# Performance work log

Hardware: AMD Instinct MI355X
Metric: run time of the kernel (lower is better)

The kernel has to match this reference:

```python
import jax, jax.numpy as jnp
import numpy as np

B, S, H = 2, 2048, 2048
E, I, K = 32, 768, 8
NORM_TOPK = True


def setup_inputs() -> dict:
    key = jax.random.key(0)
    k0, k1, k2, k3, k4 = jax.random.split(key, 5)
    scale = 0.02
    return {
        "hidden_states": jax.random.normal(k0, (B, S, H), dtype=jnp.float32),
        "w_router": jax.random.normal(k1, (E, H), dtype=jnp.float32) * scale,   # gate.weight [E,H]
        "w_gate": jax.random.normal(k2, (E, I, H), dtype=jnp.float32) * scale,  # gate_proj per expert
        "w_up": jax.random.normal(k3, (E, I, H), dtype=jnp.float32) * scale,    # up_proj per expert
        "w_down": jax.random.normal(k4, (E, H, I), dtype=jnp.float32) * scale,  # down_proj per expert
    }


def reference(hidden_states, w_router, w_gate, w_up, w_down):
    b, s, h = hidden_states.shape
    x = hidden_states.reshape(-1, h)                       # [T, H]
    T = x.shape[0]

    router_logits = x @ w_router.T                         # [T, E]
    probs = jax.nn.softmax(router_logits.astype(jnp.float32), axis=-1)
    topk_w, topk_idx = jax.lax.top_k(probs, K)             # [T, K]
    if NORM_TOPK:
        topk_w = topk_w / jnp.sum(topk_w, axis=-1, keepdims=True)

    # Scatter top-k weights into a dense combine matrix [T, E]
    combine = jnp.zeros((T, w_router.shape[0]), dtype=jnp.float32)
    combine = combine.at[jnp.arange(T)[:, None], topk_idx].add(topk_w)

    # SwiGLU MLP per expert, combined with routing weights
    g = jnp.einsum('th,eih->tei', x, w_gate)               # [T, E, I]
    u = jnp.einsum('th,eih->tei', x, w_up)                 # [T, E, I]
    act = jax.nn.silu(g) * u                               # [T, E, I]
    act = act * combine[:, :, None]                        # weight before down-proj
    out = jnp.einsum('tei,ehi->th', act, w_down)           # [T, H]

    out = out.reshape(b, s, h).astype(hidden_states.dtype)
    return out, router_logits.reshape(b, s, -1)
```

## Files before the change

kernel.cpp:

```cpp
#include <hip/hip_runtime.h>
#include <hip/hip_bf16.h>

#define T_TOK 4096
#define H_DIM 2048
#define E_EXP 32
#define I_DIM 768
#define K_TOP 8
#define TOTAL_ROWS (T_TOK * K_TOP)

typedef __attribute__((ext_vector_type(8))) short bfrag;
typedef __attribute__((ext_vector_type(4))) float f32x4;

static __device__ __forceinline__ unsigned short f2bf(float f) {
  unsigned int x = __float_as_uint(f);
  x += 0x7FFFu + ((x >> 16) & 1u);
  return (unsigned short)(x >> 16);
}
static __device__ __forceinline__ unsigned int pack2(float a, float b) {
  return (unsigned int)f2bf(a) | ((unsigned int)f2bf(b) << 16);
}

#if __has_builtin(__builtin_amdgcn_global_load_lds)
typedef __attribute__((address_space(1))) const unsigned int as1_u32;
typedef __attribute__((address_space(3))) unsigned int as3_u32;
static __device__ __forceinline__ void gll16(const unsigned short* g, unsigned short* l) {
  __builtin_amdgcn_global_load_lds((as1_u32*)g, (as3_u32*)l, 16, 0, 0);
}
#else
static __device__ __forceinline__ void gll16(const unsigned short* g, unsigned short* l) {
  uint4 v = *(const uint4*)g;
  ((uint4*)l)[threadIdx.x & 63] = v;
}
#endif

__global__ __launch_bounds__(256) void cast_f32_bf16_kernel(const float* __restrict__ s,
                                                            unsigned short* __restrict__ d,
                                                            long long n8) {
  long long i = (long long)blockIdx.x * 256 + threadIdx.x;
  if (i >= n8) return;
  const float4* sp = (const float4*)s;
  float4 a = sp[2 * i], b = sp[2 * i + 1];
  uint4 o;
  o.x = pack2(a.x, a.y); o.y = pack2(a.z, a.w);
  o.z = pack2(b.x, b.y); o.w = pack2(b.z, b.w);
  ((uint4*)d)[i] = o;
}

__global__ __launch_bounds__(256) void router_kernel(
    const float* __restrict__ x, const float* __restrict__ wr,
    float* __restrict__ logits_out, int* __restrict__ tok_list,
    float* __restrict__ wgt_list, int* __restrict__ cnt) {
  __shared__ float xs[4][H_DIM];
  __shared__ float lg[4][E_EXP];
  const int tid = threadIdx.x;
  const int t0 = blockIdx.x * 4;

  const float4* src = (const float4*)(x + (size_t)t0 * H_DIM);
  float4* dst = (float4*)&xs[0][0];
  for (int i = tid; i < 4 * H_DIM / 4; i += 256) dst[i] = src[i];
  __syncthreads();

  const int g = tid >> 3, l8 = tid & 7;
  float a0 = 0.f, a1 = 0.f, a2 = 0.f, a3 = 0.f;
  const float* w = wr + (size_t)g * H_DIM;
  for (int c = l8; c < H_DIM; c += 8) {
    float wv = w[c];
    a0 += xs[0][c] * wv; a1 += xs[1][c] * wv;
    a2 += xs[2][c] * wv; a3 += xs[3][c] * wv;
  }
  #pragma unroll
  for (int m = 4; m; m >>= 1) {
    a0 += __shfl_xor(a0, m); a1 += __shfl_xor(a1, m);
    a2 += __shfl_xor(a2, m); a3 += __shfl_xor(a3, m);
  }
  if (l8 == 0) { lg[0][g] = a0; lg[1][g] = a1; lg[2][g] = a2; lg[3][g] = a3; }
  __syncthreads();

  if (tid < 128) {
    int r = tid >> 5, e = tid & 31;
    logits_out[(size_t)(t0 + r) * E_EXP + e] = lg[r][e];
  }

  if (tid < 4) {
    int t = t0 + tid;
    unsigned sel = 0;
    float lv[K_TOP]; int ei[K_TOP];
    #pragma unroll
    for (int k = 0; k < K_TOP; ++k) {
      float best = -3.4e38f; int bi = 0;
      for (int e = 0; e < E_EXP; ++e) {
        float v = lg[tid][e];
        if (!((sel >> e) & 1u) && v > best) { best = v; bi = e; }
      }
      sel |= 1u << bi; lv[k] = best; ei[k] = bi;
    }
    float m = lv[0], se = 0.f, ex[K_TOP];
    #pragma unroll
    for (int k = 0; k < K_TOP; ++k) { ex[k] = __expf(lv[k] - m); se += ex[k]; }
    float inv = 1.f / se;
    #pragma unroll
    for (int k = 0; k < K_TOP; ++k) {
      int e = ei[k];
      int pos = atomicAdd(&cnt[e], 1);
      tok_list[e * T_TOK + pos] = t;
      wgt_list[e * T_TOK + pos] = ex[k] * inv;
    }
  }
}

__global__ void scan_kernel(const int* __restrict__ cnt, int* __restrict__ aoff) {
  if (threadIdx.x == 0 && blockIdx.x == 0) {
    int s = 0;
    for (int e = 0; e < E_EXP; ++e) { aoff[e] = s; s += cnt[e]; }
  }
}


__global__ __launch_bounds__(256) void gateup_kernel(
    const unsigned short* __restrict__ xb,
    const unsigned short* __restrict__ wgb, const unsigned short* __restrict__ wub,
    const int* __restrict__ cnt, const int* __restrict__ aoff,
    const int* __restrict__ tok_list, const float* __restrict__ wgt_list,
    unsigned short* __restrict__ act) {
  const int bx = blockIdx.x;
  const int cb = bx % 6;
  const int t  = bx / 6;
  const int e  = t >> 5, rb = t & 31;
  const int nt = cnt[e];
  const int row0 = rb * 128;
  if (row0 >= nt) return;
  const int n0 = cb * 128;

  __shared__ __align__(16) unsigned short As[128 * 64];
  __shared__ __align__(16) unsigned short Bgs[128 * 64];
  __shared__ __align__(16) unsigned short Bus[128 * 64];
  __shared__ int toks[128];
  __shared__ float wrow[128];

  const int tid = threadIdx.x;
  if (tid < 128) {
    int r = row0 + tid;
    bool v = r < nt;
    toks[tid] = v ? tok_list[e * T_TOK + r] : 0;
    wrow[tid] = v ? wgt_list[e * T_TOK + r] : 0.f;
  }
  __syncthreads();

  const int rr = tid >> 3, c8 = tid & 7;
  const unsigned short* pa[4];
  const unsigned short* pbg[4];
  #pragma unroll
  for (int j = 0; j < 4; ++j) {
    int r = j * 32 + rr;
    int c = 8 * (c8 ^ (r & 7));
    pa[j]  = xb + (size_t)toks[r] * H_DIM + c;
    pbg[j] = wgb + ((size_t)e * I_DIM + n0 + r) * H_DIM + c;
  }
  const size_t du = (size_t)(wub - wgb);

  f32x4 zero = {0.f, 0.f, 0.f, 0.f};
  f32x4 ag[4][4], au[4][4];
  #pragma unroll
  for (int m = 0; m < 4; ++m)
    #pragma unroll
    for (int n = 0; n < 4; ++n) { ag[m][n] = zero; au[m][n] = zero; }

  const int lane = tid & 63;
  const int w = tid >> 6;
  const int wr = (w >> 1) * 64, wc = (w & 1) * 64;
  const int lbase = w * 512;

  for (int kt = 0; kt < H_DIM; kt += 64) {
    #pragma unroll
    for (int j = 0; j < 4; ++j) gll16(pa[j] + kt,       &As[j * 2048 + lbase]);
    #pragma unroll
    for (int j = 0; j < 4; ++j) gll16(pbg[j] + kt,      &Bgs[j * 2048 + lbase]);
    #pragma unroll
    for (int j = 0; j < 4; ++j) gll16(pbg[j] + du + kt, &Bus[j * 2048 + lbase]);
    __syncthreads();
    #pragma unroll
    for (int kk = 0; kk < 2; ++kk) {
      bfrag a[4], bg[4], bu[4];
      #pragma unroll
      for (int m = 0; m < 4; ++m) {
        int r = wr + m * 16 + (lane & 15);
        int el = (r * 64 + kk * 32 + (lane >> 4) * 8) ^ ((r & 7) << 3);
        a[m] = *(const bfrag*)&As[el];
      }
      #pragma unroll
      for (int n = 0; n < 4; ++n) {
        int r = wc + n * 16 + (lane & 15);
        int el = (r * 64 + kk * 32 + (lane >> 4) * 8) ^ ((r & 7) << 3);
        bg[n] = *(const bfrag*)&Bgs[el];
        bu[n] = *(const bfrag*)&Bus[el];
      }
      #pragma unroll
      for (int m = 0; m < 4; ++m)
        #pragma unroll
        for (int n = 0; n < 4; ++n) {
          ag[m][n] = __builtin_amdgcn_mfma_f32_16x16x32_bf16(a[m], bg[n], ag[m][n], 0, 0, 0);
          au[m][n] = __builtin_amdgcn_mfma_f32_16x16x32_bf16(a[m], bu[n], au[m][n], 0, 0, 0);
        }
    }
    __syncthreads();
  }

  const int aoe = aoff[e];
  #pragma unroll
  for (int m = 0; m < 4; ++m) {
    #pragma unroll
    for (int r4 = 0; r4 < 4; ++r4) {
      int rloc = wr + m * 16 + (lane >> 4) * 4 + r4;
      int grow = row0 + rloc;
      if (grow < nt) {
        float wgt = wrow[rloc];
        size_t base = (size_t)(aoe + grow) * I_DIM + n0 + wc + (lane & 15);
        #pragma unroll
        for (int n = 0; n < 4; ++n) {
          float g = ag[m][n][r4], u = au[m][n][r4];
          float s = g / (1.f + __expf(-g));
          act[base + n * 16] = f2bf(s * u * wgt);
        }
      }
    }
  }
}

__global__ __launch_bounds__(256) void down_kernel(
    const unsigned short* __restrict__ act, const unsigned short* __restrict__ wdb,
    const int* __restrict__ cnt, const int* __restrict__ aoff,
    const int* __restrict__ tok_list, float* __restrict__ out) {
  const int bx = blockIdx.x;
  const int cb = bx & 15;
  const int t  = bx >> 4;
  const int e  = t >> 5, rb = t & 31;
  const int nt = cnt[e];
  const int row0 = rb * 128;
  if (row0 >= nt) return;
  const int h0 = cb * 128;

  __shared__ __align__(16) unsigned short As[128 * 64];
  __shared__ __align__(16) unsigned short Bd[128 * 64];
  __shared__ int toks[128];

  const int tid = threadIdx.x;
  const int aoe = aoff[e];
  if (tid < 128) {
    int r = row0 + tid;
    toks[tid] = (r < nt) ? tok_list[e * T_TOK + r] : 0;
  }
  __syncthreads();

  const int rr = tid >> 3, c8 = tid & 7;
  const unsigned short* pa[4];
  const unsigned short* pb[4];
  #pragma unroll
  for (int j = 0; j < 4; ++j) {
    int r = j * 32 + rr;
    int c = 8 * (c8 ^ (r & 7));
    int arow = aoe + row0 + r;
    if (arow > TOTAL_ROWS - 1) arow = TOTAL_ROWS - 1;
    pa[j] = act + (size_t)arow * I_DIM + c;
    pb[j] = wdb + ((size_t)e * H_DIM + h0 + r) * I_DIM + c;
  }

  f32x4 zero = {0.f, 0.f, 0.f, 0.f};
  f32x4 acc[4][4];
  #pragma unroll
  for (int m = 0; m < 4; ++m)
    #pragma unroll
    for (int n = 0; n < 4; ++n) acc[m][n] = zero;

  const int lane = tid & 63;
  const int w = tid >> 6;
  const int wr = (w >> 1) * 64, wc = (w & 1) * 64;
  const int lbase = w * 512;

  for (int kt = 0; kt < I_DIM; kt += 64) {
    #pragma unroll
    for (int j = 0; j < 4; ++j) gll16(pa[j] + kt, &As[j * 2048 + lbase]);
    #pragma unroll
    for (int j = 0; j < 4; ++j) gll16(pb[j] + kt, &Bd[j * 2048 + lbase]);
    __syncthreads();
    #pragma unroll
    for (int kk = 0; kk < 2; ++kk) {
      bfrag a[4], b[4];
      #pragma unroll
      for (int m = 0; m < 4; ++m) {
        int r = wr + m * 16 + (lane & 15);
        int el = (r * 64 + kk * 32 + (lane >> 4) * 8) ^ ((r & 7) << 3);
        a[m] = *(const bfrag*)&As[el];
      }
      #pragma unroll
      for (int n = 0; n < 4; ++n) {
        int r = wc + n * 16 + (lane & 15);
        int el = (r * 64 + kk * 32 + (lane >> 4) * 8) ^ ((r & 7) << 3);
        b[n] = *(const bfrag*)&Bd[el];
      }
      #pragma unroll
      for (int m = 0; m < 4; ++m)
        #pragma unroll
        for (int n = 0; n < 4; ++n)
          acc[m][n] = __builtin_amdgcn_mfma_f32_16x16x32_bf16(a[m], b[n], acc[m][n], 0, 0, 0);
    }
    __syncthreads();
  }

  #pragma unroll
  for (int m = 0; m < 4; ++m) {
    #pragma unroll
    for (int r4 = 0; r4 < 4; ++r4) {
      int rloc = wr + m * 16 + (lane >> 4) * 4 + r4;
      int grow = row0 + rloc;
      if (grow < nt) {
        int tok = toks[rloc];
        size_t base = (size_t)tok * H_DIM + h0 + wc + (lane & 15);
        #pragma unroll
        for (int n = 0; n < 4; ++n)
          atomicAdd(out + base + n * 16, acc[m][n][r4]);
      }
    }
  }
}

__global__ __launch_bounds__(256) void gateup_fb(
    const unsigned short* __restrict__ xb,
    const float* __restrict__ wg, const float* __restrict__ wu,
    const int* __restrict__ cnt, const int* __restrict__ aoff,
    const int* __restrict__ tok_list, const float* __restrict__ wgt_list,
    unsigned short* __restrict__ act) {
  const int e = blockIdx.x >> 5;
  const int rb = blockIdx.x & 31;
  const int nt = cnt[e];
  const int row0 = rb * 128;
  if (row0 >= nt) return;
  const int n0 = blockIdx.y * 128;

  __shared__ __align__(16) unsigned short As[128 * 64];
  __shared__ __align__(16) unsigned short Bgs[128 * 64];
  __shared__ __align__(16) unsigned short Bus[128 * 64];
  __shared__ int toks[128];
  __shared__ float wrow[128];

  const int tid = threadIdx.x;
  if (tid < 128) {
    int r = row0 + tid;
    bool v = r < nt;
    toks[tid] = v ? tok_list[e * T_TOK + r] : 0;
    wrow[tid] = v ? wgt_list[e * T_TOK + r] : 0.f;
  }

  f32x4 zero = {0.f, 0.f, 0.f, 0.f};
  f32x4 ag[4][4], au[4][4];
  #pragma unroll
  for (int m = 0; m < 4; ++m)
    #pragma unroll
    for (int n = 0; n < 4; ++n) { ag[m][n] = zero; au[m][n] = zero; }

  const int lane = tid & 63;
  const int wv = tid >> 6;
  const int wr = (wv >> 1) * 64;
  const int wc = (wv & 1) * 64;

  const float* wgp = wg + ((size_t)e * I_DIM + n0) * H_DIM;
  const float* wup = wu + ((size_t)e * I_DIM + n0) * H_DIM;

  for (int kt = 0; kt < H_DIM; kt += 64) {
    __syncthreads();
    #pragma unroll
    for (int i = 0; i < 4; ++i) {
      int q = tid + 256 * i;
      int r = q >> 3, cc = q & 7;
      uint4 av = *(const uint4*)(xb + (size_t)toks[r] * H_DIM + (kt + cc * 8));
      int el = (r * 64 + cc * 8) ^ ((r & 7) << 3);
      *(uint4*)&As[el] = av;
    }
    #pragma unroll
    for (int i = 0; i < 4; ++i) {
      int q = tid + 256 * i;
      int r = q >> 3, cc = q & 7;
      size_t off = (size_t)r * H_DIM + (kt + cc * 8);
      float4 g0 = *(const float4*)(wgp + off);
      float4 g1 = *(const float4*)(wgp + off + 4);
      float4 u0 = *(const float4*)(wup + off);
      float4 u1 = *(const float4*)(wup + off + 4);
      int el = (r * 64 + cc * 8) ^ ((r & 7) << 3);
      uint4 pg, pu;
      pg.x = pack2(g0.x, g0.y); pg.y = pack2(g0.z, g0.w);
      pg.z = pack2(g1.x, g1.y); pg.w = pack2(g1.z, g1.w);
      pu.x = pack2(u0.x, u0.y); pu.y = pack2(u0.z, u0.w);
      pu.z = pack2(u1.x, u1.y); pu.w = pack2(u1.z, u1.w);
      *(uint4*)&Bgs[el] = pg;
      *(uint4*)&Bus[el] = pu;
    }
    __syncthreads();
    #pragma unroll
    for (int kk = 0; kk < 2; ++kk) {
      bfrag a[4], bg[4], bu[4];
      #pragma unroll
      for (int m = 0; m < 4; ++m) {
        int r = wr + m * 16 + (lane & 15);
        int el = (r * 64 + kk * 32 + (lane >> 4) * 8) ^ ((r & 7) << 3);
        a[m] = *(const bfrag*)&As[el];
      }
      #pragma unroll
      for (int n = 0; n < 4; ++n) {
        int r = wc + n * 16 + (lane & 15);
        int el = (r * 64 + kk * 32 + (lane >> 4) * 8) ^ ((r & 7) << 3);
        bg[n] = *(const bfrag*)&Bgs[el];
        bu[n] = *(const bfrag*)&Bus[el];
      }
      #pragma unroll
      for (int m = 0; m < 4; ++m)
        #pragma unroll
        for (int n = 0; n < 4; ++n) {
          ag[m][n] = __builtin_amdgcn_mfma_f32_16x16x32_bf16(a[m], bg[n], ag[m][n], 0, 0, 0);
          au[m][n] = __builtin_amdgcn_mfma_f32_16x16x32_bf16(a[m], bu[n], au[m][n], 0, 0, 0);
        }
    }
  }

  const int aoe = aoff[e];
  #pragma unroll
  for (int m = 0; m < 4; ++m) {
    #pragma unroll
    for (int r4 = 0; r4 < 4; ++r4) {
      int rloc = wr + m * 16 + (lane >> 4) * 4 + r4;
      int grow = row0 + rloc;
      if (grow < nt) {
        float wgt = wrow[rloc];
        size_t base = (size_t)(aoe + grow) * I_DIM + n0 + wc + (lane & 15);
        #pragma unroll
        for (int n = 0; n < 4; ++n) {
          float g = ag[m][n][r4];
          float u = au[m][n][r4];
          float s = g / (1.f + __expf(-g));
          act[base + n * 16] = f2bf(s * u * wgt);
        }
      }
    }
  }
}

__global__ __launch_bounds__(256) void down_fb(
    const unsigned short* __restrict__ act, const float* __restrict__ wd,
    const int* __restrict__ cnt, const int* __restrict__ aoff,
    const int* __restrict__ tok_list, float* __restrict__ out) {
  const int e = blockIdx.x >> 5;
  const int rb = blockIdx.x & 31;
  const int nt = cnt[e];
  const int row0 = rb * 128;
  if (row0 >= nt) return;
  const int h0 = blockIdx.y * 128;

  __shared__ __align__(16) unsigned short As[128 * 64];
  __shared__ __align__(16) unsigned short Bd[128 * 64];
  __shared__ int toks[128];

  const int tid = threadIdx.x;
  const int aoe = aoff[e];
  if (tid < 128) {
    int r = row0 + tid;
    toks[tid] = (r < nt) ? tok_list[e * T_TOK + r] : 0;
  }

  f32x4 zero = {0.f, 0.f, 0.f, 0.f};
  f32x4 acc[4][4];
  #pragma unroll
  for (int m = 0; m < 4; ++m)
    #pragma unroll
    for (int n = 0; n < 4; ++n) acc[m][n] = zero;

  const int lane = tid & 63;
  const int wv = tid >> 6;
  const int wr = (wv >> 1) * 64;
  const int wc = (wv & 1) * 64;

  const float* wdp = wd + ((size_t)e * H_DIM + h0) * I_DIM;

  for (int kt = 0; kt < I_DIM; kt += 64) {
    __syncthreads();
    #pragma unroll
    for (int i = 0; i < 4; ++i) {
      int q = tid + 256 * i;
      int r = q >> 3, cc = q & 7;
      int arow = aoe + row0 + r;
      if (arow > TOTAL_ROWS - 1) arow = TOTAL_ROWS - 1;
      uint4 av = *(const uint4*)(act + (size_t)arow * I_DIM + (kt + cc * 8));
      int el = (r * 64 + cc * 8) ^ ((r & 7) << 3);
      *(uint4*)&As[el] = av;
    }
    #pragma unroll
    for (int i = 0; i < 4; ++i) {
      int q = tid + 256 * i;
      int r = q >> 3, cc = q & 7;
      size_t off = (size_t)r * I_DIM + (kt + cc * 8);
      float4 b0 = *(const float4*)(wdp + off);
      float4 b1 = *(const float4*)(wdp + off + 4);
      int el = (r * 64 + cc * 8) ^ ((r & 7) << 3);
      uint4 pb;
      pb.x = pack2(b0.x, b0.y); pb.y = pack2(b0.z, b0.w);
      pb.z = pack2(b1.x, b1.y); pb.w = pack2(b1.z, b1.w);
      *(uint4*)&Bd[el] = pb;
    }
    __syncthreads();
    #pragma unroll
    for (int kk = 0; kk < 2; ++kk) {
      bfrag a[4], b[4];
      #pragma unroll
      for (int m = 0; m < 4; ++m) {
        int r = wr + m * 16 + (lane & 15);
        int el = (r * 64 + kk * 32 + (lane >> 4) * 8) ^ ((r & 7) << 3);
        a[m] = *(const bfrag*)&As[el];
      }
      #pragma unroll
      for (int n = 0; n < 4; ++n) {
        int r = wc + n * 16 + (lane & 15);
        int el = (r * 64 + kk * 32 + (lane >> 4) * 8) ^ ((r & 7) << 3);
        b[n] = *(const bfrag*)&Bd[el];
      }
      #pragma unroll
      for (int m = 0; m < 4; ++m)
        #pragma unroll
        for (int n = 0; n < 4; ++n)
          acc[m][n] = __builtin_amdgcn_mfma_f32_16x16x32_bf16(a[m], b[n], acc[m][n], 0, 0, 0);
    }
  }

  #pragma unroll
  for (int m = 0; m < 4; ++m) {
    #pragma unroll
    for (int r4 = 0; r4 < 4; ++r4) {
      int rloc = wr + m * 16 + (lane >> 4) * 4 + r4;
      int grow = row0 + rloc;
      if (grow < nt) {
        int tok = toks[rloc];
        size_t base = (size_t)tok * H_DIM + h0 + wc + (lane & 15);
        #pragma unroll
        for (int n = 0; n < 4; ++n)
          atomicAdd(out + base + n * 16, acc[m][n][r4]);
      }
    }
  }
}

extern "C" void kernel_launch(void* const* d_in, const int* in_sizes, int n_in,
                              void* d_out, int out_size, void* d_ws, size_t ws_size,
                              hipStream_t stream) {
  const float* x  = (const float*)d_in[0];
  const float* wr = (const float*)d_in[1];
  const float* wg = (const float*)d_in[2];
  const float* wu = (const float*)d_in[3];
  const float* wd = (const float*)d_in[4];
  float* out = (float*)d_out;
  float* logits_out = out + (size_t)T_TOK * H_DIM;

  const long long WELEM = (long long)E_EXP * I_DIM * H_DIM;
  const size_t WBYT = (size_t)WELEM * 2;

  const size_t XB_OFF  = 0;
  const size_t WGB_OFF = 16777216;
  const size_t WUB_OFF = WGB_OFF + WBYT;
  const size_t WDB_OFF = WUB_OFF + WBYT;
  const size_t TOK_OFF = WDB_OFF + WBYT;
  const size_t WGT_OFF = TOK_OFF + 524288;
  const size_t CNT_OFF = WGT_OFF + 524288;
  const size_t AOF_OFF = CNT_OFF + 256;
  const size_t ACT_OFF = AOF_OFF + 256;
  const size_t NEED    = ACT_OFF + (size_t)TOTAL_ROWS * I_DIM * 2;

  char* ws = (char*)d_ws;
  hipMemsetAsync(out, 0, (size_t)T_TOK * H_DIM * sizeof(float), stream);

  if (ws_size >= NEED) {
    unsigned short* xb  = (unsigned short*)(ws + XB_OFF);
    unsigned short* wgb = (unsigned short*)(ws + WGB_OFF);
    unsigned short* wub = (unsigned short*)(ws + WUB_OFF);
    unsigned short* wdb = (unsigned short*)(ws + WDB_OFF);
    int*   tok_list = (int*)(ws + TOK_OFF);
    float* wgt_list = (float*)(ws + WGT_OFF);
    int*   cnt  = (int*)(ws + CNT_OFF);
    int*   aoff = (int*)(ws + AOF_OFF);
    unsigned short* act = (unsigned short*)(ws + ACT_OFF);

    hipMemsetAsync(cnt, 0, 256, stream);
    cast_f32_bf16_kernel<<<4096, 256, 0, stream>>>(x, xb, (long long)T_TOK * H_DIM / 8);
    cast_f32_bf16_kernel<<<24576, 256, 0, stream>>>(wg, wgb, WELEM / 8);
    cast_f32_bf16_kernel<<<24576, 256, 0, stream>>>(wu, wub, WELEM / 8);
    cast_f32_bf16_kernel<<<24576, 256, 0, stream>>>(wd, wdb, WELEM / 8);
    router_kernel<<<T_TOK / 4, 256, 0, stream>>>(x, wr, logits_out, tok_list, wgt_list, cnt);
    scan_kernel<<<1, 64, 0, stream>>>(cnt, aoff);
    gateup_kernel<<<E_EXP * 32 * 6, 256, 0, stream>>>(
        xb, wgb, wub, cnt, aoff, tok_list, wgt_list, act);
    down_kernel<<<E_EXP * 32 * 16, 256, 0, stream>>>(
        act, wdb, cnt, aoff, tok_list, out);
  } else {
    unsigned short* xb   = (unsigned short*)ws;
    int*   tok_list      = (int*)(ws + 16777216);
    float* wgt_list      = (float*)(ws + 16777216 + 524288);
    int*   cnt           = (int*)(ws + 16777216 + 1048576);
    int*   aoff          = (int*)(ws + 16777216 + 1048576 + 256);
    unsigned short* act  = (unsigned short*)(ws + 16777216 + 1048576 + 512);

    hipMemsetAsync(cnt, 0, 256, stream);
    cast_f32_bf16_kernel<<<4096, 256, 0, stream>>>(x, xb, (long long)T_TOK * H_DIM / 8);
    router_kernel<<<T_TOK / 4, 256, 0, stream>>>(x, wr, logits_out, tok_list, wgt_list, cnt);
    scan_kernel<<<1, 64, 0, stream>>>(cnt, aoff);
    gateup_fb<<<dim3(E_EXP * 32, I_DIM / 128), 256, 0, stream>>>(
        xb, wg, wu, cnt, aoff, tok_list, wgt_list, act);
    down_fb<<<dim3(E_EXP * 32, H_DIM / 128), 256, 0, stream>>>(
        act, wd, cnt, aoff, tok_list, out);
  }
}
```

Baseline: 1.483 ms.

## Double-buffer LDS in MoE GEMMs, shrink gate-up N tile, reorder block mapping

After: 2.315 ms. 56.1% more time.

```diff
diff --git a/kernel.cpp b/kernel.cpp
--- a/kernel.cpp
+++ b/kernel.cpp
@@ -123,86 +123,91 @@
     const int* __restrict__ tok_list, const float* __restrict__ wgt_list,
     unsigned short* __restrict__ act) {
   const int bx = blockIdx.x;
-  const int cb = bx % 6;
-  const int t  = bx / 6;
-  const int e  = t >> 5, rb = t & 31;
+  const int rb = bx & 31;
+  const int q  = bx >> 5;
+  const int cb = q % 12;
+  const int e  = q / 12;
   const int nt = cnt[e];
   const int row0 = rb * 128;
   if (row0 >= nt) return;
-  const int n0 = cb * 128;
-
-  __shared__ __align__(16) unsigned short As[128 * 64];
-  __shared__ __align__(16) unsigned short Bgs[128 * 64];
-  __shared__ __align__(16) unsigned short Bus[128 * 64];
-  __shared__ int toks[128];
-  __shared__ float wrow[128];
+  const int n0 = cb * 64;
+
+  __shared__ __align__(16) unsigned short lds[2][16384];
 
   const int tid = threadIdx.x;
-  if (tid < 128) {
-    int r = row0 + tid;
-    bool v = r < nt;
-    toks[tid] = v ? tok_list[e * T_TOK + r] : 0;
-    wrow[tid] = v ? wgt_list[e * T_TOK + r] : 0.f;
-  }
-  __syncthreads();
-
   const int rr = tid >> 3, c8 = tid & 7;
+
   const unsigned short* pa[4];
-  const unsigned short* pbg[4];
+  const unsigned short* pbg[2];
   #pragma unroll
   for (int j = 0; j < 4; ++j) {
     int r = j * 32 + rr;
-    int c = 8 * (c8 ^ (r & 7));
-    pa[j]  = xb + (size_t)toks[r] * H_DIM + c;
-    pbg[j] = wgb + ((size_t)e * I_DIM + n0 + r) * H_DIM + c;
+    int gr = row0 + r;
+    int tok = (gr < nt) ? tok_list[e * T_TOK + gr] : 0;
+    pa[j] = xb + (size_t)tok * H_DIM + 8 * (c8 ^ (r & 7));
+  }
+  #pragma unroll
+  for (int j = 0; j < 2; ++j) {
+    int r = j * 32 + rr;
+    pbg[j] = wgb + ((size_t)e * I_DIM + n0 + r) * H_DIM + 8 * (c8 ^ (r & 7));
   }
   const size_t du = (size_t)(wub - wgb);
 
   f32x4 zero = {0.f, 0.f, 0.f, 0.f};
-  f32x4 ag[4][4], au[4][4];
+  f32x4 ag[4][2], au[4][2];
   #pragma unroll
   for (int m = 0; m < 4; ++m)
     #pragma unroll
-    for (int n = 0; n < 4; ++n) { ag[m][n] = zero; au[m][n] = zero; }
+    for (int n = 0; n < 2; ++n) { ag[m][n] = zero; au[m][n] = zero; }
 
   const int lane = tid & 63;
   const int w = tid >> 6;
-  const int wr = (w >> 1) * 64, wc = (w & 1) * 64;
+  const int wr = (w >> 1) * 64;
+  const int wc = (w & 1) * 32;
   const int lbase = w * 512;
 
+  auto STAGE = [&](int b, int kt) {
+    #pragma unroll
+    for (int j = 0; j < 4; ++j) gll16(pa[j] + kt,       &lds[b][j * 2048 + lbase]);
+    #pragma unroll
+    for (int j = 0; j < 2; ++j) gll16(pbg[j] + kt,      &lds[b][8192 + j * 2048 + lbase]);
+    #pragma unroll
+    for (int j = 0; j < 2; ++j) gll16(pbg[j] + du + kt, &lds[b][12288 + j * 2048 + lbase]);
+  };
+
+  int cur = 0;
+  STAGE(0, 0);
+  __syncthreads();
+
   for (int kt = 0; kt < H_DIM; kt += 64) {
-    #pragma unroll
-    for (int j = 0; j < 4; ++j) gll16(pa[j] + kt,       &As[j * 2048 + lbase]);
-    #pragma unroll
-    for (int j = 0; j < 4; ++j) gll16(pbg[j] + kt,      &Bgs[j * 2048 + lbase]);
-    #pragma unroll
-    for (int j = 0; j < 4; ++j) gll16(pbg[j] + du + kt, &Bus[j * 2048 + lbase]);
-    __syncthreads();
+    int nxt = kt + 64;
+    if (nxt < H_DIM) STAGE(cur ^ 1, nxt);
     #pragma unroll
     for (int kk = 0; kk < 2; ++kk) {
-      bfrag a[4], bg[4], bu[4];
+      bfrag a[4], bg[2], bu[2];
       #pragma unroll
       for (int m = 0; m < 4; ++m) {
         int r = wr + m * 16 + (lane & 15);
         int el = (r * 64 + kk * 32 + (lane >> 4) * 8) ^ ((r & 7) << 3);
-        a[m] = *(const bfrag*)&As[el];
-      }
-      #pragma unroll
-      for (int n = 0; n < 4; ++n) {
+        a[m] = *(const bfrag*)&lds[cur][el];
+      }
+      #pragma unroll
+      for (int n = 0; n < 2; ++n) {
         int r = wc + n * 16 + (lane & 15);
         int el = (r * 64 + kk * 32 + (lane >> 4) * 8) ^ ((r & 7) << 3);
-        bg[n] = *(const bfrag*)&Bgs[el];
-        bu[n] = *(const bfrag*)&Bus[el];
+        bg[n] = *(const bfrag*)&lds[cur][8192 + el];
+        bu[n] = *(const bfrag*)&lds[cur][12288 + el];
       }
       #pragma unroll
       for (int m = 0; m < 4; ++m)
         #pragma unroll
-        for (int n = 0; n < 4; ++n) {
+        for (int n = 0; n < 2; ++n) {
           ag[m][n] = __builtin_amdgcn_mfma_f32_16x16x32_bf16(a[m], bg[n], ag[m][n], 0, 0, 0);
           au[m][n] = __builtin_amdgcn_mfma_f32_16x16x32_bf16(a[m], bu[n], au[m][n], 0, 0, 0);
         }
     }
     __syncthreads();
+    cur ^= 1;
   }
 
   const int aoe = aoff[e];
@@ -213,10 +218,10 @@
       int rloc = wr + m * 16 + (lane >> 4) * 4 + r4;
       int grow = row0 + rloc;
       if (grow < nt) {
-        float wgt = wrow[rloc];
+        float wgt = wgt_list[e * T_TOK + grow];
         size_t base = (size_t)(aoe + grow) * I_DIM + n0 + wc + (lane & 15);
         #pragma unroll
-        for (int n = 0; n < 4; ++n) {
+        for (int n = 0; n < 2; ++n) {
           float g = ag[m][n][r4], u = au[m][n][r4];
           float s = g / (1.f + __expf(-g));
           act[base + n * 16] = f2bf(s * u * wgt);
@@ -231,27 +236,21 @@
     const int* __restrict__ cnt, const int* __restrict__ aoff,
     const int* __restrict__ tok_list, float* __restrict__ out) {
   const int bx = blockIdx.x;
-  const int cb = bx & 15;
-  const int t  = bx >> 4;
-  const int e  = t >> 5, rb = t & 31;
+  const int rb = bx & 31;
+  const int q  = bx >> 5;
+  const int cb = q & 15;
+  const int e  = q >> 4;
   const int nt = cnt[e];
   const int row0 = rb * 128;
   if (row0 >= nt) return;
   const int h0 = cb * 128;
 
-  __shared__ __align__(16) unsigned short As[128 * 64];
-  __shared__ __align__(16) unsigned short Bd[128 * 64];
-  __shared__ int toks[128];
+  __shared__ __align__(16) unsigned short lds[2][16384];
 
   const int tid = threadIdx.x;
   const int aoe = aoff[e];
-  if (tid < 128) {
-    int r = row0 + tid;
-    toks[tid] = (r < nt) ? tok_list[e * T_TOK + r] : 0;
-  }
-  __syncthreads();
-
   const int rr = tid >> 3, c8 = tid & 7;
+
   const unsigned short* pa[4];
   const unsigned short* pb[4];
   #pragma unroll
@@ -276,12 +275,20 @@
   const int wr = (w >> 1) * 64, wc = (w & 1) * 64;
   const int lbase = w * 512;
 
+  auto STAGE = [&](int b, int kt) {
+    #pragma unroll
+    for (int j = 0; j < 4; ++j) gll16(pa[j] + kt, &lds[b][j * 2048 + lbase]);
+    #pragma unroll
+    for (int j = 0; j < 4; ++j) gll16(pb[j] + kt, &lds[b][8192 + j * 2048 + lbase]);
+  };
+
+  int cur = 0;
+  STAGE(0, 0);
+  __syncthreads();
+
   for (int kt = 0; kt < I_DIM; kt += 64) {
-    #pragma unroll
-    for (int j = 0; j < 4; ++j) gll16(pa[j] + kt, &As[j * 2048 + lbase]);
-    #pragma unroll
-    for (int j = 0; j < 4; ++j) gll16(pb[j] + kt, &Bd[j * 2048 + lbase]);
-    __syncthreads();
+    int nxt = kt + 64;
+    if (nxt < I_DIM) STAGE(cur ^ 1, nxt);
     #pragma unroll
     for (int kk = 0; kk < 2; ++kk) {
       bfrag a[4], b[4];
@@ -289,13 +296,13 @@
       for (int m = 0; m < 4; ++m) {
         int r = wr + m * 16 + (lane & 15);
         int el = (r * 64 + kk * 32 + (lane >> 4) * 8) ^ ((r & 7) << 3);
-        a[m] = *(const bfrag*)&As[el];
+        a[m] = *(const bfrag*)&lds[cur][el];
       }
       #pragma unroll
       for (int n = 0; n < 4; ++n) {
         int r = wc + n * 16 + (lane & 15);
         int el = (r * 64 + kk * 32 + (lane >> 4) * 8) ^ ((r & 7) << 3);
-        b[n] = *(const bfrag*)&Bd[el];
+        b[n] = *(const bfrag*)&lds[cur][8192 + el];
       }
       #pragma unroll
       for (int m = 0; m < 4; ++m)
@@ -304,6 +311,7 @@
           acc[m][n] = __builtin_amdgcn_mfma_f32_16x16x32_bf16(a[m], b[n], acc[m][n], 0, 0, 0);
     }
     __syncthreads();
+    cur ^= 1;
   }
 
   #pragma unroll
@@ -313,7 +321,7 @@
       int rloc = wr + m * 16 + (lane >> 4) * 4 + r4;
       int grow = row0 + rloc;
       if (grow < nt) {
-        int tok = toks[rloc];
+        int tok = tok_list[e * T_TOK + grow];
         size_t base = (size_t)tok * H_DIM + h0 + wc + (lane & 15);
         #pragma unroll
         for (int n = 0; n < 4; ++n)
@@ -590,9 +598,9 @@
     cast_f32_bf16_kernel<<<24576, 256, 0, stream>>>(wd, wdb, WELEM / 8);
     router_kernel<<<T_TOK / 4, 256, 0, stream>>>(x, wr, logits_out, tok_list, wgt_list, cnt);
     scan_kernel<<<1, 64, 0, stream>>>(cnt, aoff);
-    gateup_kernel<<<E_EXP * 32 * 6, 256, 0, stream>>>(
+    gateup_kernel<<<E_EXP * 12 * 32, 256, 0, stream>>>(
         xb, wgb, wub, cnt, aoff, tok_list, wgt_list, act);
-    down_kernel<<<E_EXP * 32 * 16, 256, 0, stream>>>(
+    down_kernel<<<E_EXP * 16 * 32, 256, 0, stream>>>(
         act, wdb, cnt, aoff, tok_list, out);
   } else {
     unsigned short* xb   = (unsigned short*)ws;
```
